# Kernel tuning notes

Measured on AMD Instinct MI355X. Metric: run time of the kernel, lower is better.

## Reference

```python
import jax, jax.numpy as jnp
import numpy as np

N = 8192          # rays
S = 128           # steps per ray (cfg.n_steps_fixed)
POS_BANDS = 10    # positional-encoding bands for positions
VD_BANDS = 4      # bands for view directions (default in _encode_viewdir)
EARLY_STOP_T = 1e-4


def pos_enc(x, num_bands):
    """[..., 3] -> [..., 3 + 2*3*num_bands], interleaved [x, sin(f*x), cos(f*x), ...]."""
    parts = [x]
    for i in range(num_bands):  # small fixed loop over frequency bands
        f = jnp.asarray(2.0 ** i, dtype=x.dtype)
        parts.append(jnp.sin(f * x))
        parts.append(jnp.cos(f * x))
    return jnp.concatenate(parts, axis=-1)


def setup_inputs() -> dict:
    key = jax.random.key(0)
    ks = jax.random.split(key, 10)
    orig = 0.1 * jax.random.normal(ks[0], (N, 3), jnp.float32)
    dirs = jax.random.normal(ks[1], (N, 3), jnp.float32)
    dirs = dirs / (jnp.linalg.norm(dirs, axis=-1, keepdims=True) + 1e-8)
    tmin = 0.5 + 0.5 * jax.random.uniform(ks[2], (N,), jnp.float32)
    tmax = tmin + 1.0 + jax.random.uniform(ks[3], (N,), jnp.float32)
    d_enc = 3 + 2 * 3 * POS_BANDS          # 63
    d_vd = 3 + 2 * 3 * VD_BANDS            # 27
    hid, feat = 64, 15
    W1 = jax.random.normal(ks[4], (d_enc, hid), jnp.float32) / np.sqrt(d_enc)
    b1 = jnp.zeros((hid,), jnp.float32)
    W2 = jax.random.normal(ks[5], (hid, 1 + feat), jnp.float32) / np.sqrt(hid)
    b2 = jnp.zeros((1 + feat,), jnp.float32)
    V1 = jax.random.normal(ks[6], (feat + d_vd, hid), jnp.float32) / np.sqrt(feat + d_vd)
    c1 = jnp.zeros((hid,), jnp.float32)
    V2 = jax.random.normal(ks[7], (hid, 3), jnp.float32) / np.sqrt(hid)
    c2 = jnp.zeros((3,), jnp.float32)
    return {"orig": orig, "dirs": dirs, "tmin": tmin, "tmax": tmax,
            "W1": W1, "b1": b1, "W2": W2, "b2": b2,
            "V1": V1, "c1": c1, "V2": V2, "c2": c2}


def reference(orig, dirs, tmin, tmax, W1, b1, W2, b2, V1, c1, V2, c2):
    # --- fixed-step sampling ---
    t_uniform = jnp.linspace(0.0, 1.0, S, dtype=jnp.float32)          # [S]
    t = tmin[:, None] + t_uniform[None, :] * (tmax - tmin)[:, None]   # [N, S]
    dt = jnp.mean(tmax - tmin) / S                                    # scalar step size

    # --- positions and encoder ---
    pos = orig[:, None, :] + dirs[:, None, :] * t[..., None]          # [N, S, 3]
    enc = pos_enc(pos, POS_BANDS)                                     # [N, S, 63]

    # --- field MLP: sigma + rgb features ---
    h = jax.nn.relu(enc @ W1 + b1)                                    # [N, S, 64]
    out = h @ W2 + b2                                                 # [N, S, 16]
    sigma = jax.nn.relu(out[..., 0])                                  # [N, S]
    rgb_feat = out[..., 1:]                                           # [N, S, 15]

    # --- rgb head with view-direction PE ---
    vd = dirs / (jnp.linalg.norm(dirs, axis=-1, keepdims=True) + 1e-8)
    vd_enc = pos_enc(vd, VD_BANDS)                                    # [N, 27]
    vd_enc = jnp.broadcast_to(vd_enc[:, None, :], (rgb_feat.shape[0], S, vd_enc.shape[-1]))
    rgb_in = jnp.concatenate([rgb_feat, vd_enc], axis=-1)             # [N, S, 42]
    rgb_steps = jax.nn.sigmoid(jax.nn.relu(rgb_in @ V1 + c1) @ V2 + c2)  # [N, S, 3]

    # --- alpha compositing with early stop (dense-masked equivalent) ---
    alpha = 1.0 - jnp.exp(-sigma * dt)                                # [N, S]
    one_minus = 1.0 - alpha
    T_excl = jnp.concatenate(
        [jnp.ones_like(alpha[:, :1]), jnp.cumprod(one_minus, axis=1)[:, :-1]], axis=1
    )                                                                 # transmittance before each step
    active = T_excl > EARLY_STOP_T                                    # ray still marching
    weights = T_excl * alpha * active                                 # [N, S]
    rgb_out = jnp.sum(weights[..., None] * rgb_steps, axis=1)         # [N, 3]
    T_out = jnp.prod(jnp.where(active, one_minus, 1.0), axis=1)       # final transmittance at stop
    return rgb_out, T_out
```

## Files before the change

### kernel.cpp

```cpp
#include <hip/hip_runtime.h>
#include <hip/hip_bf16.h>

#define NRAYS 8192
#define SAMP  128
#define DVD   27
#define NFEAT 15

typedef float  f32x4  __attribute__((ext_vector_type(4)));
typedef short  short8 __attribute__((ext_vector_type(8)));
typedef unsigned int u32x2 __attribute__((ext_vector_type(2)));
typedef unsigned int u32x4 __attribute__((ext_vector_type(4)));

#define IMG_W1   0
#define IMG_C    4608
#define IMG_W2S  9216
#define IMG_V2   10368
#define IMG_SHORTS 11520
#define GVC_OFF  23040

static __device__ __forceinline__ void stbf(short* p, float x) {
    union { unsigned u; struct { short lo, hi; } s; } v;
    v.u = __float_as_uint(x) + 0x8000u;
    *p = v.s.hi;
}
static __device__ __forceinline__ float bf2f(short s) {
    return __uint_as_float(((unsigned)(unsigned short)s) << 16);
}
static __device__ __forceinline__ unsigned pk2bf(float lo, float hi) {
    unsigned r;
    asm("v_cvt_pk_bf16_f32 %0, %1, %2" : "=v"(r) : "v"(lo), "v"(hi));
    return r;
}
static __device__ __forceinline__ float sin_fast(float x) {
    float r = x * 0.15915494309189535f;
    r = r - floorf(r);
    return __builtin_amdgcn_sinf(r);
}
static __device__ __forceinline__ float cos_fast(float x) {
    float r = x * 0.15915494309189535f;
    r = r - floorf(r);
    return __builtin_amdgcn_cosf(r);
}

static __device__ __forceinline__ int kmap(int r) {
    if (r == 0) return 30;
    if (r == 1) return 31;
    if (r == 2) return 62;
    const int q = r - 3, i = q / 6, c = q - 6 * i;
    return (i < 5 ? 6 * i : 32 + 6 * (i - 5)) + c;
}

__global__ void __launch_bounds__(256)
prep_kernel(const float* __restrict__ W1, const float* __restrict__ b1,
            const float* __restrict__ W2, const float* __restrict__ b2,
            const float* __restrict__ V1, const float* __restrict__ c1,
            const float* __restrict__ V2, short* __restrict__ img,
            float* __restrict__ gvc) {
    const int g = blockIdx.x * 256 + threadIdx.x;
    if (g < 4032) {
        const int r = g >> 6, n = g & 63;
        stbf(&img[IMG_W1 + n * 72 + kmap(r)], W1[g]);
    } else if (g < 4096) {
        const int n = g - 4032;
        stbf(&img[IMG_W1 + n * 72 + 63], b1[n]);
    } else {
        const int i = g - 4096;
        const int k = i >> 6, n = i & 63;
        float a = 0.0f;
        #pragma unroll
        for (int j = 0; j < 15; j++) a += W2[k * 16 + 1 + j] * V1[j * 64 + n];
        stbf(&img[IMG_C + n * 72 + k], a);
    }
    if (g < 64) {
        stbf(&img[IMG_W2S + g], W2[g * 16]);
    } else if (g < 256) {
        const int i = g - 64, k = i / 3, n = i - 3 * k;
        stbf(&img[IMG_V2 + n * 72 + k], V2[i]);
    } else if (g < 320) {
        const int n = g - 256;
        float a = c1[n];
        #pragma unroll
        for (int j = 0; j < 15; j++) a += b2[1 + j] * V1[j * 64 + n];
        gvc[n] = a;
    } else if (g < 1600) {
        const int z = g - 320, row = z >> 3, c = z & 7;
        int base;
        if (row < 64)       base = IMG_W1  + row * 72;
        else if (row < 128) base = IMG_C   + (row - 64) * 72;
        else if (row < 144) base = IMG_W2S + (row - 128) * 72;
        else                base = IMG_V2  + (row - 144) * 72;
        img[base + 64 + c] = 0;
    } else if (g < 2560) {
        const int z = g - 1600, n = 1 + (z >> 6), k = z & 63;
        img[IMG_W2S + n * 72 + k] = 0;
    } else if (g < 3392) {
        const int z = g - 2560, n = 3 + (z >> 6), k = z & 63;
        img[IMG_V2 + n * 72 + k] = 0;
    }
}

#define SMEM_BYTES 37840

__global__ void __launch_bounds__(256, 4)
march_kernel(const float* __restrict__ orig,
             const float* __restrict__ dirs,
             const float* __restrict__ tmin,
             const float* __restrict__ tmax,
             const float* __restrict__ b2,
             const float* __restrict__ c2,
             const float* __restrict__ V1,
             const short* __restrict__ img,
             const float* __restrict__ gvc,
             float* __restrict__ out) {
    __shared__ __align__(16) char smem[SMEM_BYTES];
    short* const sW1t = (short*)(smem);
    short* const sEa  = (short*)(smem);
    short* const sCt  = (short*)(smem + 18432);
    short* const sW2s = (short*)(smem + 27648);
    short* const sV2t = (short*)(smem + 29952);
    float* const sOm  = (float*)(smem + 32256);
    short* const sRgb = (short*)(smem + 34304);
    float* const sVde = (float*)(smem + 37376);
    float* const sRed = (float*)(smem + 37824);

    const int tid  = threadIdx.x;
    const int lane = tid & 63;
    const int wave = tid >> 6;
    const int ray  = blockIdx.x * 4 + wave;

    {
        const float4* tm0 = (const float4*)tmin;
        const float4* tm1 = (const float4*)tmax;
        float s = 0.0f;
        #pragma unroll
        for (int it = 0; it < 8; it++) {
            const int i = tid + it * 256;
            const float4 a = tm1[i], b = tm0[i];
            s += (a.x - b.x) + (a.y - b.y) + (a.z - b.z) + (a.w - b.w);
        }
        #pragma unroll
        for (int off = 32; off > 0; off >>= 1)
            s += __shfl_xor(s, off, 64);
        if (lane == 0) sRed[wave] = s;
    }

    {
        const u32x4* src = (const u32x4*)img;
        u32x4* dst = (u32x4*)smem;
        #pragma unroll
        for (int it = 0; it < 6; it++) {
            const int i = tid + it * 256;
            if (i < 1440) {
                const int d = (i < 576) ? i : i + 576;
                dst[d] = src[i];
            }
        }
    }

    const float ox = orig[ray * 3 + 0];
    const float oy = orig[ray * 3 + 1];
    const float oz = orig[ray * 3 + 2];
    const float dx = dirs[ray * 3 + 0];
    const float dy = dirs[ray * 3 + 1];
    const float dz = dirs[ray * 3 + 2];
    const float t0v = tmin[ray];
    const float trange = tmax[ray] - t0v;

    {
        const float nrm = sqrtf(dx * dx + dy * dy + dz * dz);
        const float inv = 1.0f / (nrm + 1e-8f);
        const float vx = dx * inv, vy = dy * inv, vz = dz * inv;
        if (lane < DVD) {
            float val;
            if (lane < 3) {
                val = (lane == 0) ? vx : ((lane == 1) ? vy : vz);
            } else {
                const int q = lane - 3;
                const int b = q / 6;
                const int r = q - 6 * b;
                const bool isSin = (r < 3);
                const int d = isSin ? r : (r - 3);
                const float comp = (d == 0) ? vx : ((d == 1) ? vy : vz);
                const float a = (float)(1 << b) * comp;
                val = isSin ? sin_fast(a) : cos_fast(a);
            }
            sVde[wave * 28 + lane] = val;
        }
    }
    __syncthreads();

    const float dtv = (sRed[0] + sRed[1] + sRed[2] + sRed[3]) *
                      (1.0f / ((float)NRAYS * (float)SAMP));

    const int nfr  = lane & 15;
    const int quad = lane >> 4;

    float gv[4];
    {
        const f32x4 g0 = *(const f32x4*)&gvc[4 * nfr];
        gv[0] = g0.x; gv[1] = g0.y; gv[2] = g0.z; gv[3] = g0.w;
    }
    #pragma unroll 9
    for (int q = 0; q < DVD; q++) {
        const float e = sVde[wave * 28 + q];
        const f32x4 vv = *(const f32x4*)&V1[(NFEAT + q) * 64 + 4 * nfr];
        gv[0] += e * vv.x; gv[1] += e * vv.y;
        gv[2] += e * vv.z; gv[3] += e * vv.w;
    }

    short8 w1f[4][2];
    #pragma unroll
    for (int nt = 0; nt < 4; nt++)
        #pragma unroll
        for (int kt = 0; kt < 2; kt++)
            w1f[nt][kt] = *(const short8*)&sW1t[(4 * nfr + nt) * 72 + quad * 8 + kt * 32];

    const float bb2 = b2[0];
    const float bc2 = (nfr < 3) ? c2[nfr] : 0.0f;

    __syncthreads();

    short* const myE = sEa + wave * (32 * 72);

    const int sl   = lane >> 1;
    const int half = lane & 1;
    const float fmul = half ? 5.0929581789406507f
                            : 0.15915494309189535f;

    #pragma unroll 1
    for (int qq = 0; qq < 4; qq++) {
        {
            const int s = qq * 32 + sl;
            const float t = t0v + (float)s * (1.0f / 127.0f) * trange;
            const float px = ox + dx * t, py = oy + dy * t, pz = oz + dz * t;
            float rx = px * fmul; rx -= floorf(rx);
            float ry = py * fmul; ry -= floorf(ry);
            float rz = pz * fmul; rz -= floorf(rz);
            float sx = __builtin_amdgcn_sinf(rx), cx = __builtin_amdgcn_cosf(rx);
            float sy = __builtin_amdgcn_sinf(ry), cy = __builtin_amdgcn_cosf(ry);
            float sz = __builtin_amdgcn_sinf(rz), cz = __builtin_amdgcn_cosf(rz);
            unsigned e[16] __attribute__((aligned(16)));
            #pragma unroll
            for (int j = 0; j < 5; j++) {
                e[3 * j + 0] = pk2bf(sx, sy);
                e[3 * j + 1] = pk2bf(sz, cx);
                e[3 * j + 2] = pk2bf(cy, cz);
                if (j < 4) {
                    const float tx = sx + sx, ty = sy + sy, tz = sz + sz;
                    const float nsx = tx * cx, nsy = ty * cy, nsz = tz * cz;
                    cx = __builtin_fmaf(-tx, sx, 1.0f);
                    cy = __builtin_fmaf(-ty, sy, 1.0f);
                    cz = __builtin_fmaf(-tz, sz, 1.0f);
                    sx = nsx; sy = nsy; sz = nsz;
                }
            }
            e[15] = half ? pk2bf(pz, 1.0f) : pk2bf(px, py);
            u32x4* dst = (u32x4*)((unsigned*)&myE[sl * 72] + 16 * half);
            dst[0] = *(const u32x4*)&e[0];
            dst[1] = *(const u32x4*)&e[4];
            dst[2] = *(const u32x4*)&e[8];
            dst[3] = *(const u32x4*)&e[12];
        }
        f32x4 acc1[2][4];
        #pragma unroll
        for (int mt = 0; mt < 2; mt++)
            #pragma unroll
            for (int nt = 0; nt < 4; nt++)
                acc1[mt][nt] = (f32x4){0.0f, 0.0f, 0.0f, 0.0f};
        {
            short8 af[2][2];
            #pragma unroll
            for (int mt = 0; mt < 2; mt++)
                #pragma unroll
                for (int kt = 0; kt < 2; kt++)
                    af[mt][kt] = *(const short8*)&myE[(nfr + 16 * mt) * 72 + quad * 8 + kt * 32];
            #pragma unroll
            for (int mt = 0; mt < 2; mt++)
                #pragma unroll
                for (int nt = 0; nt < 4; nt++)
                    #pragma unroll
                    for (int kt = 0; kt < 2; kt++)
                        acc1[mt][nt] = __builtin_amdgcn_mfma_f32_16x16x32_bf16(
                            af[mt][kt], w1f[nt][kt], acc1[mt][nt], 0, 0, 0);
        }
        #pragma unroll
        for (int mt = 0; mt < 2; mt++)
            #pragma unroll
            for (int r = 0; r < 4; r++) {
                const int m = 4 * quad + r + 16 * mt;
                u32x2 hp;
                hp.x = pk2bf(fmaxf(acc1[mt][0][r], 0.0f),
                             fmaxf(acc1[mt][1][r], 0.0f));
                hp.y = pk2bf(fmaxf(acc1[mt][2][r], 0.0f),
                             fmaxf(acc1[mt][3][r], 0.0f));
                *(u32x2*)&myE[m * 72 + 4 * nfr] = hp;
            }
        short8 ah[2][2];
        #pragma unroll
        for (int mt = 0; mt < 2; mt++)
            #pragma unroll
            for (int kt = 0; kt < 2; kt++)
                ah[mt][kt] = *(const short8*)&myE[(nfr + 16 * mt) * 72 + quad * 8 + kt * 32];
        {
            f32x4 acc2[2];
            acc2[0] = (f32x4){bb2, bb2, bb2, bb2};
            acc2[1] = (f32x4){bb2, bb2, bb2, bb2};
            short8 w2sf[2];
            #pragma unroll
            for (int kt = 0; kt < 2; kt++)
                w2sf[kt] = *(const short8*)&sW2s[nfr * 72 + quad * 8 + kt * 32];
            #pragma unroll
            for (int mt = 0; mt < 2; mt++)
                #pragma unroll
                for (int kt = 0; kt < 2; kt++)
                    acc2[mt] = __builtin_amdgcn_mfma_f32_16x16x32_bf16(
                        ah[mt][kt], w2sf[kt], acc2[mt], 0, 0, 0);
            if (nfr == 0) {
                #pragma unroll
                for (int mt = 0; mt < 2; mt++)
                    #pragma unroll
                    for (int r = 0; r < 4; r++) {
                        const int m = 4 * quad + r + 16 * mt;
                        const float sg = fmaxf(acc2[mt][r], 0.0f);
                        sOm[wave * 128 + qq * 32 + m] = __expf(-sg * dtv);
                    }
            }
        }
        #pragma unroll
        for (int nth = 0; nth < 2; nth++) {
            f32x4 acc3[2][2];
            #pragma unroll
            for (int mt = 0; mt < 2; mt++)
                #pragma unroll
                for (int j = 0; j < 2; j++) {
                    const float gvi = gv[2 * nth + j];
                    acc3[mt][j] = (f32x4){gvi, gvi, gvi, gvi};
                }
            #pragma unroll
            for (int j = 0; j < 2; j++)
                #pragma unroll
                for (int kt = 0; kt < 2; kt++) {
                    const short8 cf = *(const short8*)
                        &sCt[(4 * nfr + 2 * nth + j) * 72 + quad * 8 + kt * 32];
                    #pragma unroll
                    for (int mt = 0; mt < 2; mt++)
                        acc3[mt][j] = __builtin_amdgcn_mfma_f32_16x16x32_bf16(
                            ah[mt][kt], cf, acc3[mt][j], 0, 0, 0);
                }
            #pragma unroll
            for (int mt = 0; mt < 2; mt++)
                #pragma unroll
                for (int r = 0; r < 4; r++) {
                    const int m = 4 * quad + r + 16 * mt;
                    *(unsigned*)&myE[m * 72 + 4 * nfr + 2 * nth] =
                        pk2bf(fmaxf(acc3[mt][0][r], 0.0f),
                              fmaxf(acc3[mt][1][r], 0.0f));
                }
        }
        {
            f32x4 acc4[2];
            acc4[0] = (f32x4){bc2, bc2, bc2, bc2};
            acc4[1] = (f32x4){bc2, bc2, bc2, bc2};
            short8 agg[2][2];
            #pragma unroll
            for (int mt = 0; mt < 2; mt++)
                #pragma unroll
                for (int kt = 0; kt < 2; kt++)
                    agg[mt][kt] = *(const short8*)&myE[(nfr + 16 * mt) * 72 + quad * 8 + kt * 32];
            short8 v2f[2];
            #pragma unroll
            for (int kt = 0; kt < 2; kt++)
                v2f[kt] = *(const short8*)&sV2t[nfr * 72 + quad * 8 + kt * 32];
            #pragma unroll
            for (int mt = 0; mt < 2; mt++)
                #pragma unroll
                for (int kt = 0; kt < 2; kt++)
                    acc4[mt] = __builtin_amdgcn_mfma_f32_16x16x32_bf16(
                        agg[mt][kt], v2f[kt], acc4[mt], 0, 0, 0);
            if (nfr < 3) {
                #pragma unroll
                for (int mt = 0; mt < 2; mt++)
                    #pragma unroll
                    for (int r = 0; r < 4; r++) {
                        const int m = 4 * quad + r + 16 * mt;
                        const float val = acc4[mt][r];
                        stbf(&sRgb[wave * 384 + (qq * 32 + m) * 3 + nfr],
                             1.0f / (1.0f + __expf(-val)));
                    }
            }
        }
    }

    const float om0 = sOm[wave * 128 + 2 * lane];
    const float om1 = sOm[wave * 128 + 2 * lane + 1];
    const float al0 = 1.0f - om0;
    const float al1 = 1.0f - om1;

    float inc = om0 * om1;
    #pragma unroll
    for (int off = 1; off < 64; off <<= 1) {
        const float q = __shfl_up(inc, off, 64);
        if (lane >= off) inc *= q;
    }
    float Texc = __shfl_up(inc, 1, 64);
    if (lane == 0) Texc = 1.0f;

    const float T0 = Texc;
    const float T1 = Texc * om0;
    const float a0 = (T0 > 1e-4f) ? 1.0f : 0.0f;
    const float a1 = (T1 > 1e-4f) ? 1.0f : 0.0f;
    const float w0 = T0 * al0 * a0;
    const float w1 = T1 * al1 * a1;

    float cr = w0 * bf2f(sRgb[wave * 384 + (2 * lane) * 3 + 0]) +
               w1 * bf2f(sRgb[wave * 384 + (2 * lane + 1) * 3 + 0]);
    float cg = w0 * bf2f(sRgb[wave * 384 + (2 * lane) * 3 + 1]) +
               w1 * bf2f(sRgb[wave * 384 + (2 * lane + 1) * 3 + 1]);
    float cb = w0 * bf2f(sRgb[wave * 384 + (2 * lane) * 3 + 2]) +
               w1 * bf2f(sRgb[wave * 384 + (2 * lane + 1) * 3 + 2]);
    float tp = (a0 > 0.0f ? om0 : 1.0f) * (a1 > 0.0f ? om1 : 1.0f);

    #pragma unroll
    for (int off = 32; off > 0; off >>= 1) {
        cr += __shfl_xor(cr, off, 64);
        cg += __shfl_xor(cg, off, 64);
        cb += __shfl_xor(cb, off, 64);
        tp *= __shfl_xor(tp, off, 64);
    }

    if (lane == 0) {
        out[ray * 3 + 0] = cr;
        out[ray * 3 + 1] = cg;
        out[ray * 3 + 2] = cb;
        out[NRAYS * 3 + ray] = tp;
    }
}

extern "C" void kernel_launch(void* const* d_in, const int* in_sizes, int n_in,
                              void* d_out, int out_size, void* d_ws, size_t ws_size,
                              hipStream_t stream) {
    const float* orig = (const float*)d_in[0];
    const float* dirs = (const float*)d_in[1];
    const float* tmin = (const float*)d_in[2];
    const float* tmax = (const float*)d_in[3];
    const float* W1   = (const float*)d_in[4];
    const float* b1   = (const float*)d_in[5];
    const float* W2   = (const float*)d_in[6];
    const float* b2   = (const float*)d_in[7];
    const float* V1   = (const float*)d_in[8];
    const float* c1   = (const float*)d_in[9];
    const float* V2   = (const float*)d_in[10];
    const float* c2   = (const float*)d_in[11];

    short* img = (short*)d_ws;
    float* gvc = (float*)((char*)d_ws + GVC_OFF);

    prep_kernel<<<32, 256, 0, stream>>>(W1, b1, W2, b2, V1, c1, V2, img, gvc);
    march_kernel<<<NRAYS / 4, 256, 0, stream>>>(orig, dirs, tmin, tmax,
                                                b2, c2, V1, img, gvc,
                                                (float*)d_out);
}
```

Measured before the change: 120.4 us.

## Replace padded LDS rows with XOR-swizzled layout and raise occupancy to five blocks

Weight and activation tiles in shared memory move from 72-short padded rows to unpadded 64-short rows with an XOR swizzle on 16-byte chunks, so bank conflicts stay avoided without the padding. The W2 sigma column and V2 rows shrink to dense vectors that lanes read by broadcast or clamped indexing instead of zero-padded 16-row tiles. This cuts LDS use from about 37.8 KB to 30.2 KB per block and raises launch bounds to 5 blocks per CU. The risks are extra address arithmetic for the swizzle and more register pressure under the tighter occupancy bound.

After: 204.4 us. 69.8% more time.

```diff
diff --git a/kernel.cpp b/kernel.cpp
--- a/kernel.cpp
+++ b/kernel.cpp
@@ -11,12 +11,15 @@
 typedef unsigned int u32x2 __attribute__((ext_vector_type(2)));
 typedef unsigned int u32x4 __attribute__((ext_vector_type(4)));
 
-#define IMG_W1   0
-#define IMG_C    4608
-#define IMG_W2S  9216
-#define IMG_V2   10368
-#define IMG_SHORTS 11520
-#define GVC_OFF  23040
+#define GVC_OFF  16896
+#define IMG_CHUNKS 1056
+
+static __device__ __forceinline__ int XB(int row, int cb) {
+    return row * 128 + (cb ^ ((row & 7) << 4));
+}
+static __device__ __forceinline__ int XS(int row, int k) {
+    return row * 64 + (k ^ ((row & 7) << 3));
+}
 
 static __device__ __forceinline__ void stbf(short* p, float x) {
     union { unsigned u; struct { short lo, hi; } s; } v;
@@ -59,49 +62,38 @@
     const int g = blockIdx.x * 256 + threadIdx.x;
     if (g < 4032) {
         const int r = g >> 6, n = g & 63;
-        stbf(&img[IMG_W1 + n * 72 + kmap(r)], W1[g]);
+        const int prow = (n & 3) * 16 + (n >> 2);
+        stbf(&img[XS(prow, kmap(r))], W1[g]);
     } else if (g < 4096) {
         const int n = g - 4032;
-        stbf(&img[IMG_W1 + n * 72 + 63], b1[n]);
-    } else {
+        const int prow = (n & 3) * 16 + (n >> 2);
+        stbf(&img[XS(prow, 63)], b1[n]);
+    } else if (g < 8192) {
         const int i = g - 4096;
         const int k = i >> 6, n = i & 63;
+        const int prow = (n & 3) * 16 + (n >> 2);
         float a = 0.0f;
         #pragma unroll
         for (int j = 0; j < 15; j++) a += W2[k * 16 + 1 + j] * V1[j * 64 + n];
-        stbf(&img[IMG_C + n * 72 + k], a);
-    }
-    if (g < 64) {
-        stbf(&img[IMG_W2S + g], W2[g * 16]);
-    } else if (g < 256) {
-        const int i = g - 64, k = i / 3, n = i - 3 * k;
-        stbf(&img[IMG_V2 + n * 72 + k], V2[i]);
-    } else if (g < 320) {
-        const int n = g - 256;
+        stbf(&img[4096 + XS(prow, k)], a);
+    } else if (g < 8256) {
+        const int k = g - 8192;
+        stbf(&img[8192 + k], W2[k * 16]);
+    } else if (g < 8448) {
+        const int i = g - 8256, c = i >> 6, k = i & 63;
+        stbf(&img[8192 + 64 + c * 64 + k], V2[k * 3 + c]);
+    } else if (g < 8512) {
+        const int n = g - 8448;
         float a = c1[n];
         #pragma unroll
         for (int j = 0; j < 15; j++) a += b2[1 + j] * V1[j * 64 + n];
         gvc[n] = a;
-    } else if (g < 1600) {
-        const int z = g - 320, row = z >> 3, c = z & 7;
-        int base;
-        if (row < 64)       base = IMG_W1  + row * 72;
-        else if (row < 128) base = IMG_C   + (row - 64) * 72;
-        else if (row < 144) base = IMG_W2S + (row - 128) * 72;
-        else                base = IMG_V2  + (row - 144) * 72;
-        img[base + 64 + c] = 0;
-    } else if (g < 2560) {
-        const int z = g - 1600, n = 1 + (z >> 6), k = z & 63;
-        img[IMG_W2S + n * 72 + k] = 0;
-    } else if (g < 3392) {
-        const int z = g - 2560, n = 3 + (z >> 6), k = z & 63;
-        img[IMG_V2 + n * 72 + k] = 0;
-    }
-}
-
-#define SMEM_BYTES 37840
-
-__global__ void __launch_bounds__(256, 4)
+    }
+}
+
+#define SMEM_BYTES 30208
+
+__global__ void __launch_bounds__(256, 5)
 march_kernel(const float* __restrict__ orig,
              const float* __restrict__ dirs,
              const float* __restrict__ tmin,
@@ -113,15 +105,13 @@
              const float* __restrict__ gvc,
              float* __restrict__ out) {
     __shared__ __align__(16) char smem[SMEM_BYTES];
-    short* const sW1t = (short*)(smem);
-    short* const sEa  = (short*)(smem);
-    short* const sCt  = (short*)(smem + 18432);
-    short* const sW2s = (short*)(smem + 27648);
-    short* const sV2t = (short*)(smem + 29952);
-    float* const sOm  = (float*)(smem + 32256);
-    short* const sRgb = (short*)(smem + 34304);
-    float* const sVde = (float*)(smem + 37376);
-    float* const sRed = (float*)(smem + 37824);
+    char*  const sEc  = smem;
+    char*  const sCtc = smem + 16384;
+    short* const sSm  = (short*)(smem + 24576);
+    float* const sOm  = (float*)(smem + 25088);
+    short* const sRgb = (short*)(smem + 27136);
+    float* const sVde = (float*)(smem + 8192);
+    float* const sRed = (float*)(smem + 8640);
 
     const int tid  = threadIdx.x;
     const int lane = tid & 63;
@@ -148,10 +138,10 @@
         const u32x4* src = (const u32x4*)img;
         u32x4* dst = (u32x4*)smem;
         #pragma unroll
-        for (int it = 0; it < 6; it++) {
+        for (int it = 0; it < 5; it++) {
             const int i = tid + it * 256;
-            if (i < 1440) {
-                const int d = (i < 576) ? i : i + 576;
+            if (i < IMG_CHUNKS) {
+                const int d = (i < 512) ? i : i + 512;
                 dst[d] = src[i];
             }
         }
@@ -194,6 +184,7 @@
 
     const int nfr  = lane & 15;
     const int quad = lane >> 4;
+    const int cbq  = quad * 16;
 
     float gv[4];
     {
@@ -213,14 +204,14 @@
     for (int nt = 0; nt < 4; nt++)
         #pragma unroll
         for (int kt = 0; kt < 2; kt++)
-            w1f[nt][kt] = *(const short8*)&sW1t[(4 * nfr + nt) * 72 + quad * 8 + kt * 32];
+            w1f[nt][kt] = *(const short8*)(sEc + XB(nt * 16 + nfr, cbq + kt * 64));
 
     const float bb2 = b2[0];
     const float bc2 = (nfr < 3) ? c2[nfr] : 0.0f;
 
     __syncthreads();
 
-    short* const myE = sEa + wave * (32 * 72);
+    char* const myE = sEc + wave * 4096;
 
     const int sl   = lane >> 1;
     const int half = lane & 1;
@@ -255,11 +246,10 @@
                 }
             }
             e[15] = half ? pk2bf(pz, 1.0f) : pk2bf(px, py);
-            u32x4* dst = (u32x4*)((unsigned*)&myE[sl * 72] + 16 * half);
-            dst[0] = *(const u32x4*)&e[0];
-            dst[1] = *(const u32x4*)&e[4];
-            dst[2] = *(const u32x4*)&e[8];
-            dst[3] = *(const u32x4*)&e[12];
+            #pragma unroll
+            for (int w = 0; w < 4; w++)
+                *(u32x4*)(myE + XB(sl, half * 64 + w * 16)) =
+                    *(const u32x4*)&e[4 * w];
         }
         f32x4 acc1[2][4];
         #pragma unroll
@@ -273,7 +263,7 @@
             for (int mt = 0; mt < 2; mt++)
                 #pragma unroll
                 for (int kt = 0; kt < 2; kt++)
-                    af[mt][kt] = *(const short8*)&myE[(nfr + 16 * mt) * 72 + quad * 8 + kt * 32];
+                    af[mt][kt] = *(const short8*)(myE + XB(nfr + 16 * mt, cbq + kt * 64));
             #pragma unroll
             for (int mt = 0; mt < 2; mt++)
                 #pragma unroll
@@ -293,14 +283,14 @@
                              fmaxf(acc1[mt][1][r], 0.0f));
                 hp.y = pk2bf(fmaxf(acc1[mt][2][r], 0.0f),
                              fmaxf(acc1[mt][3][r], 0.0f));
-                *(u32x2*)&myE[m * 72 + 4 * nfr] = hp;
+                *(u32x2*)(myE + XB(m, 8 * nfr)) = hp;
             }
         short8 ah[2][2];
         #pragma unroll
         for (int mt = 0; mt < 2; mt++)
             #pragma unroll
             for (int kt = 0; kt < 2; kt++)
-                ah[mt][kt] = *(const short8*)&myE[(nfr + 16 * mt) * 72 + quad * 8 + kt * 32];
+                ah[mt][kt] = *(const short8*)(myE + XB(nfr + 16 * mt, cbq + kt * 64));
         {
             f32x4 acc2[2];
             acc2[0] = (f32x4){bb2, bb2, bb2, bb2};
@@ -308,7 +298,7 @@
             short8 w2sf[2];
             #pragma unroll
             for (int kt = 0; kt < 2; kt++)
-                w2sf[kt] = *(const short8*)&sW2s[nfr * 72 + quad * 8 + kt * 32];
+                w2sf[kt] = *(const short8*)&sSm[quad * 8 + kt * 32];
             #pragma unroll
             for (int mt = 0; mt < 2; mt++)
                 #pragma unroll
@@ -341,7 +331,7 @@
                 #pragma unroll
                 for (int kt = 0; kt < 2; kt++) {
                     const short8 cf = *(const short8*)
-                        &sCt[(4 * nfr + 2 * nth + j) * 72 + quad * 8 + kt * 32];
+                        (sCtc + XB((2 * nth + j) * 16 + nfr, cbq + kt * 64));
                     #pragma unroll
                     for (int mt = 0; mt < 2; mt++)
                         acc3[mt][j] = __builtin_amdgcn_mfma_f32_16x16x32_bf16(
@@ -352,7 +342,7 @@
                 #pragma unroll
                 for (int r = 0; r < 4; r++) {
                     const int m = 4 * quad + r + 16 * mt;
-                    *(unsigned*)&myE[m * 72 + 4 * nfr + 2 * nth] =
+                    *(unsigned*)(myE + XB(m, 8 * nfr + 4 * nth)) =
                         pk2bf(fmaxf(acc3[mt][0][r], 0.0f),
                               fmaxf(acc3[mt][1][r], 0.0f));
                 }
@@ -366,11 +356,12 @@
             for (int mt = 0; mt < 2; mt++)
                 #pragma unroll
                 for (int kt = 0; kt < 2; kt++)
-                    agg[mt][kt] = *(const short8*)&myE[(nfr + 16 * mt) * 72 + quad * 8 + kt * 32];
+                    agg[mt][kt] = *(const short8*)(myE + XB(nfr + 16 * mt, cbq + kt * 64));
+            const int vr = 1 + ((nfr < 3) ? nfr : 2);
             short8 v2f[2];
             #pragma unroll
             for (int kt = 0; kt < 2; kt++)
-                v2f[kt] = *(const short8*)&sV2t[nfr * 72 + quad * 8 + kt * 32];
+                v2f[kt] = *(const short8*)&sSm[vr * 64 + quad * 8 + kt * 32];
             #pragma unroll
             for (int mt = 0; mt < 2; mt++)
                 #pragma unroll
@@ -455,7 +446,7 @@
     short* img = (short*)d_ws;
     float* gvc = (float*)((char*)d_ws + GVC_OFF);
 
-    prep_kernel<<<32, 256, 0, stream>>>(W1, b1, W2, b2, V1, c1, V2, img, gvc);
+    prep_kernel<<<34, 256, 0, stream>>>(W1, b1, W2, b2, V1, c1, V2, img, gvc);
     march_kernel<<<NRAYS / 4, 256, 0, stream>>>(orig, dirs, tmin, tmax,
                                                 b2, c2, V1, img, gvc,
                                                 (float*)d_out);
```
